# Performance work log

Hardware: AMD Instinct MI355X
Metric: run time of the kernel (lower is better)

The kernel has to match this reference:

```python
import jax, jax.numpy as jnp
import numpy as np

EC = 32        # pos-embed channels per coordinate (gno_embed_channels)
MAXP = 10000.0 # gno_embed_max_positions


def sin_embed(c):
    # c: [N, D] coords in [0,1] -> [N, D*EC] transformer-style sinusoidal embedding
    half = EC // 2
    freqs = MAXP ** (jnp.arange(half, dtype=jnp.float32) / half)
    ang = c[..., None] * freqs                       # [N, D, half]
    emb = jnp.concatenate([jnp.sin(ang), jnp.cos(ang)], axis=-1)  # [N, D, EC]
    return emb.reshape(c.shape[0], -1)


def mlp(h, layers):
    n = len(layers)
    for i, (W, b) in enumerate(layers):
        h = h @ W + b
        if i < n - 1:
            h = jax.nn.gelu(h)
    return h


def gno(y, xq, f_y, idx, layers, lift, reduction):
    # y: [n_y,3] source coords, xq: [n_x,3] query coords, f_y: [n_y,C_f], idx: [n_x,K]
    ye, xe = sin_embed(y), sin_embed(xq)
    K = idx.shape[1]
    ef = jnp.concatenate(
        [ye[idx], jnp.broadcast_to(xe[:, None, :], (xq.shape[0], K, xe.shape[-1]))], axis=-1)
    k = mlp(ef, layers)                              # [n_x, K, C] kernel values
    f = f_y if lift is None else f_y @ lift[0] + lift[1]
    msg = k * f[idx]                                 # gathered features modulated by kernel
    return msg.mean(axis=1) if reduction == 'mean' else msg.sum(axis=1)


def spectral_conv(v, w):
    # v: [1,X,Y,Z,C]; w: [4,m,m,m,C,C,2] (4 corner blocks, real/imag stacked)
    m = w.shape[2]
    wc = w[..., 0] + 1j * w[..., 1]
    vf = jnp.fft.rfftn(v, axes=(1, 2, 3))
    out = jnp.zeros_like(vf)
    corners = [(slice(0, m), slice(0, m)), (slice(0, m), slice(-m, None)),
               (slice(-m, None), slice(0, m)), (slice(-m, None), slice(-m, None))]
    for i, (sx, sy) in enumerate(corners):
        blk = jnp.einsum('bxyzi,xyzio->bxyzo', vf[:, sx, sy, :m, :], wc[i])
        out = out.at[:, sx, sy, :m, :].set(blk)
    return jnp.fft.irfftn(out, s=v.shape[1:4], axes=(1, 2, 3))


def _forward(input_geom, latent_queries, output_queries, x,
             in_lift_w, in_lift_b,
             in_k_w0, in_k_b0, in_k_w1, in_k_b1, in_k_w2, in_k_b2, in_k_w3, in_k_b3,
             lift_w0, lift_b0, lift_w1, lift_b1,
             spec_w, skip_w, gate_w, gate_b, cmlp_w0, cmlp_b0, cmlp_w1, cmlp_b1,
             out_k_w0, out_k_b0, out_k_w1, out_k_b1, out_k_w2, out_k_b2,
             proj_w0, proj_b0, proj_w1, proj_b1,
             in_idx, out_idx):
    grid = latent_queries.shape[:-1]
    flat_lq = latent_queries.reshape(-1, latent_queries.shape[-1])
    # --- input GNO: point cloud -> latent grid (mean reduction) ---
    in_layers = [(in_k_w0, in_k_b0), (in_k_w1, in_k_b1), (in_k_w2, in_k_b2), (in_k_w3, in_k_b3)]
    in_p = gno(input_geom, flat_lq, x, in_idx, in_layers, (in_lift_w, in_lift_b), 'mean')
    h = in_p.reshape((1,) + grid + (in_p.shape[-1],))
    # --- lifting ChannelMLP (2 layers) ---
    h = jax.nn.gelu(h @ lift_w0 + lift_b0) @ lift_w1 + lift_b1
    # --- FNO blocks ---
    for l in range(spec_w.shape[0]):
        v_fno = spectral_conv(h, spec_w[l])
        v_skip = h @ skip_w[l]                       # linear skip
        a = jax.nn.gelu(v_fno + v_skip)
        gate = a * gate_w[l] + gate_b[l]             # soft-gating skip
        m_ = jax.nn.gelu(a @ cmlp_w0[l] + cmlp_b0[l]) @ cmlp_w1[l] + cmlp_b1[l]
        h = jax.nn.gelu(m_ + gate)
    x_latent = h.reshape(-1, h.shape[-1])            # [nx*ny*nz, C]
    # --- output GNO: latent grid -> output queries (sum reduction) ---
    out_layers = [(out_k_w0, out_k_b0), (out_k_w1, out_k_b1), (out_k_w2, out_k_b2)]
    out_eval = gno(flat_lq, output_queries, x_latent, out_idx, out_layers, None, 'sum')
    out = out_eval[None]                             # [1, n_out, C]
    # --- projection ChannelMLP ---
    return jax.nn.gelu(out @ proj_w0 + proj_b0) @ proj_w1 + proj_b1


def setup_inputs() -> dict:
    key = jax.random.key(0)
    ks = jax.random.split(key, 24)
    N_IN, N_OUT, G, K = 100000, 30000, 32, 10
    C_IN, H = 3, 64
    KIN = 2 * 3 * EC  # 192: concat of two per-point embeddings

    def w(k, shape, fan):
        return jax.random.normal(k, shape, jnp.float32) / np.sqrt(fan)

    lin = jnp.linspace(0.0, 1.0, G)
    gx, gy, gz = jnp.meshgrid(lin, lin, lin, indexing='ij')
    d = {
        'input_geom': jax.random.uniform(ks[0], (N_IN, 3), jnp.float32),
        'latent_queries': jnp.stack([gx, gy, gz], axis=-1),
        'output_queries': jax.random.uniform(ks[1], (N_OUT, 3), jnp.float32),
        'x': jax.random.normal(ks[2], (N_IN, C_IN), jnp.float32),
        'in_lift_w': w(ks[3], (C_IN, H), C_IN), 'in_lift_b': jnp.zeros((H,)),
        'in_k_w0': w(ks[4], (KIN, 80), KIN), 'in_k_b0': jnp.zeros((80,)),
        'in_k_w1': w(ks[5], (80, 80), 80), 'in_k_b1': jnp.zeros((80,)),
        'in_k_w2': w(ks[6], (80, 80), 80), 'in_k_b2': jnp.zeros((80,)),
        'in_k_w3': w(ks[7], (80, H), 80), 'in_k_b3': jnp.zeros((H,)),
        'lift_w0': w(ks[8], (H, 128), H), 'lift_b0': jnp.zeros((128,)),
        'lift_w1': w(ks[9], (128, H), 128), 'lift_b1': jnp.zeros((H,)),
        'spec_w': jax.random.normal(ks[10], (4, 4, 8, 8, 8, H, H, 2), jnp.float32) * 0.02,
        'skip_w': w(ks[11], (4, H, H), H),
        'gate_w': jnp.ones((4, H)), 'gate_b': jnp.zeros((4, H)),
        'cmlp_w0': w(ks[12], (4, H, 128), H), 'cmlp_b0': jnp.zeros((4, 128)),
        'cmlp_w1': w(ks[13], (4, 128, H), 128), 'cmlp_b1': jnp.zeros((4, H)),
        'out_k_w0': w(ks[14], (KIN, 512), KIN), 'out_k_b0': jnp.zeros((512,)),
        'out_k_w1': w(ks[15], (512, 256), 512), 'out_k_b1': jnp.zeros((256,)),
        'out_k_w2': w(ks[16], (256, H), 256), 'out_k_b2': jnp.zeros((H,)),
        'proj_w0': w(ks[17], (H, 256), H), 'proj_b0': jnp.zeros((256,)),
        'proj_w1': w(ks[18], (256, 1), 256), 'proj_b1': jnp.zeros((1,)),
        'in_idx': jax.random.randint(ks[19], (G ** 3, K), 0, N_IN),
        'out_idx': jax.random.randint(ks[20], (N_OUT, K), 0, G ** 3),
    }
    return d


def reference(input_geom, latent_queries, output_queries, x,
              in_lift_w, in_lift_b,
              in_k_w0, in_k_b0, in_k_w1, in_k_b1, in_k_w2, in_k_b2, in_k_w3, in_k_b3,
              lift_w0, lift_b0, lift_w1, lift_b1,
              spec_w, skip_w, gate_w, gate_b, cmlp_w0, cmlp_b0, cmlp_w1, cmlp_b1,
              out_k_w0, out_k_b0, out_k_w1, out_k_b1, out_k_w2, out_k_b2,
              proj_w0, proj_b0, proj_w1, proj_b1,
              in_idx, out_idx):
    return _forward(input_geom, latent_queries, output_queries, x,
                    in_lift_w, in_lift_b,
                    in_k_w0, in_k_b0, in_k_w1, in_k_b1, in_k_w2, in_k_b2, in_k_w3, in_k_b3,
                    lift_w0, lift_b0, lift_w1, lift_b1,
                    spec_w, skip_w, gate_w, gate_b, cmlp_w0, cmlp_b0, cmlp_w1, cmlp_b1,
                    out_k_w0, out_k_b0, out_k_w1, out_k_b1, out_k_w2, out_k_b2,
                    proj_w0, proj_b0, proj_w1, proj_b1,
                    in_idx, out_idx)
```

## Files before the change

kernel.cpp:

```cpp
#include <hip/hip_runtime.h>
#include <math.h>

#define N_IN   100000
#define N_LQ   32768
#define N_OUT  30000
#define KNB    10

typedef _Float16 h8 __attribute__((ext_vector_type(8)));
typedef _Float16 h4 __attribute__((ext_vector_type(4)));
typedef float    v4f __attribute__((ext_vector_type(4)));

__device__ __forceinline__ float gelu_f(float x){
  float t = 0.79788456080286536f * (x + 0.044715f*x*x*x);
  t = fminf(fmaxf(t, -15.f), 15.f);
  float e = __expf(2.f*t);
  float th = __fdividef(e - 1.f, e + 1.f);
  return 0.5f*x*(1.f + th);
}

__global__ void k_twiddle(float* __restrict__ twc, float* __restrict__ tws){
  int t = threadIdx.x;
  if(t < 32){
    double a = (double)t * 0.19634954084936207;
    twc[t] = (float)cos(a);
    tws[t] = (float)sin(a);
  }
}

__global__ void k_prep(const float* __restrict__ okw1, const float* __restrict__ okw2,
                       const float* __restrict__ ikw1, const float* __restrict__ ikw2,
                       const float* __restrict__ ikw3,
                       _Float16* W1h, _Float16* W1l, _Float16* W2h, _Float16* W2l,
                       _Float16* I1h, _Float16* I1l, _Float16* I2h, _Float16* I2l,
                       _Float16* I3h, _Float16* I3l)
{
  int idx = blockIdx.x*256 + threadIdx.x;
  if(idx < 512*256){
    int k = idx>>8, n = idx&255;
    float v = okw1[idx];
    _Float16 hi = (_Float16)v;
    W1h[n*512+k] = hi; W1l[n*512+k] = (_Float16)((v-(float)hi)*2048.f);
  }
  if(idx < 256*64){
    int k = idx>>6, n = idx&63;
    float v = okw2[idx];
    _Float16 hi = (_Float16)v;
    W2h[n*256+k] = hi; W2l[n*256+k] = (_Float16)((v-(float)hi)*2048.f);
  }
  if(idx < 6400){
    int n = idx/80, k = idx - n*80;
    float v = ikw1[k*80+n];
    _Float16 hi = (_Float16)v;
    I1h[n*80+k] = hi; I1l[n*80+k] = (_Float16)((v-(float)hi)*2048.f);
    float v2 = ikw2[k*80+n];
    _Float16 hi2 = (_Float16)v2;
    I2h[n*80+k] = hi2; I2l[n*80+k] = (_Float16)((v2-(float)hi2)*2048.f);
  }
  if(idx < 5120){
    int n = idx/80, k = idx - n*80;
    float v = ikw3[k*64+n];
    _Float16 hi = (_Float16)v;
    I3h[n*80+k] = hi; I3l[n*80+k] = (_Float16)((v-(float)hi)*2048.f);
  }
}

__global__ void k_lift_in(const float* __restrict__ x, const float* __restrict__ w,
                          const float* __restrict__ b, float* __restrict__ f){
  int i = blockIdx.x*256 + threadIdx.x;
  if(i >= N_IN*64) return;
  int p = i>>6, c = i&63;
  float v = b[c];
  v = fmaf(x[p*3+0], w[c],      v);
  v = fmaf(x[p*3+1], w[64+c],   v);
  v = fmaf(x[p*3+2], w[128+c],  v);
  f[i] = v;
}

template<int COLS, bool BIAS>
__global__ __launch_bounds__(256) void k_embed_partial(
    const float* __restrict__ coords, int npts,
    const float* __restrict__ W, int roff,
    const float* __restrict__ bias, float* __restrict__ outp)
{
  __shared__ float emb[96*8];
  int p0 = blockIdx.x*8;
  int t  = threadIdx.x;
  for(int w = t; w < 384; w += 256){
    int pl = w / 48, s = w - pl*48;
    int d = s >> 4, fi = s & 15;
    int p = p0 + pl;
    float cd = (p < npts) ? coords[(size_t)p*3 + d] : 0.f;
    double f = exp((double)fi * 0.5756462732485115);
    double a = (double)cd * f;
    double sn, cs; sincos(a, &sn, &cs);
    emb[((d<<5)+fi)*8 + pl]      = (float)sn;
    emb[((d<<5)+16+fi)*8 + pl]   = (float)cs;
  }
  __syncthreads();
  for(int c = t; c < COLS; c += 256){
    float acc[8];
    float bb = BIAS ? bias[c] : 0.f;
    #pragma unroll
    for(int u=0;u<8;u++) acc[u] = bb;
    for(int i=0;i<96;i++){
      float wv = W[(size_t)(roff+i)*COLS + c];
      const float* ep = &emb[i*8];
      float4 e0 = *(const float4*)ep;
      float4 e1 = *(const float4*)(ep+4);
      acc[0]=fmaf(e0.x,wv,acc[0]); acc[1]=fmaf(e0.y,wv,acc[1]);
      acc[2]=fmaf(e0.z,wv,acc[2]); acc[3]=fmaf(e0.w,wv,acc[3]);
      acc[4]=fmaf(e1.x,wv,acc[4]); acc[5]=fmaf(e1.y,wv,acc[5]);
      acc[6]=fmaf(e1.z,wv,acc[6]); acc[7]=fmaf(e1.w,wv,acc[7]);
    }
    #pragma unroll
    for(int u=0;u<8;u++){
      int p = p0+u;
      if(p < npts) outp[(size_t)p*COLS + c] = acc[u];
    }
  }
}

#define GI_HAHI 0
#define GI_HALO 5632
#define GI_WHI  11264
#define GI_WLO  14464
__global__ __launch_bounds__(256,2) void k_gino(
    const float* __restrict__ Ain, const float* __restrict__ Bin,
    const float* __restrict__ f_in, const int* __restrict__ iidx,
    const _Float16* __restrict__ I1h, const _Float16* __restrict__ I1l, const float* __restrict__ b1,
    const _Float16* __restrict__ I2h, const _Float16* __restrict__ I2l, const float* __restrict__ b2,
    const _Float16* __restrict__ I3h, const _Float16* __restrict__ I3l, const float* __restrict__ b3,
    float* __restrict__ in_p)
{
  __shared__ _Float16 SG[17664];
  __shared__ int js[64]; __shared__ int qs[64];
  int t = threadIdx.x;
  int wid = t>>6, lane = t&63, quad = lane>>4, lm = lane&15;
  int et0 = blockIdx.x*64;
  if(t<64){ js[t] = iidx[et0+t]; qs[t] = (et0+t)/KNB; }
  __syncthreads();

  {
    int e = t>>2, k4 = t&3;
    size_t ja = (size_t)js[e]*80, qa = (size_t)qs[e]*80;
    #pragma unroll
    for(int u=0;u<3;u++){
      int kl = k4*8 + u*32;
      if(kl < 80){
        float4 a0 = *(const float4*)(Ain + ja + kl);
        float4 a1 = *(const float4*)(Ain + ja + kl + 4);
        float4 c0 = *(const float4*)(Bin + qa + kl);
        float4 c1 = *(const float4*)(Bin + qa + kl + 4);
        float vv[8] = {a0.x+c0.x, a0.y+c0.y, a0.z+c0.z, a0.w+c0.w,
                       a1.x+c1.x, a1.y+c1.y, a1.z+c1.z, a1.w+c1.w};
        h8 hh, ll;
        #pragma unroll
        for(int q8=0;q8<8;q8++){
          float g = gelu_f(vv[q8]);
          _Float16 hi = (_Float16)g;
          hh[q8] = hi; ll[q8] = (_Float16)((g-(float)hi)*2048.f);
        }
        *(h8*)&SG[GI_HAHI + e*88 + kl] = hh;
        *(h8*)&SG[GI_HALO + e*88 + kl] = ll;
      }
    }
  }

  const float inv = 4.8828125e-4f;
  const _Float16* whp[3] = {I1h, I2h, I3h};
  const _Float16* wlp[3] = {I1l, I2l, I3l};
  const float*    bsp[3] = {b1, b2, b3};
  v4f aH[5], aL[5];

  for(int l=0;l<3;l++){
    int NT = (l==2)?4:5;
    const _Float16* wh = whp[l];
    const _Float16* wl = wlp[l];
    #pragma unroll
    for(int n=0;n<5;n++){ aH[n] = (v4f)(0.f); aL[n] = (v4f)(0.f); }
    for(int c=0;c<3;c++){
      int kb = c*32;
      int per = (c==2)?2:4;
      int units = NT*16*per;
      __syncthreads();
      for(int u=t; u<units; u+=256){
        int n = u/per, kh = (u - n*per)*8;
        float4 rh = *(const float4*)(wh + n*80 + kb + kh);
        float4 rl = *(const float4*)(wl + n*80 + kb + kh);
        *(float4*)&SG[GI_WHI + n*40 + kh] = rh;
        *(float4*)&SG[GI_WLO + n*40 + kh] = rl;
      }
      __syncthreads();
      int arow = (wid*16+lm)*88;
      if(c<2){
        h8 ah = *(const h8*)&SG[GI_HAHI + arow + kb + quad*8];
        h8 al = *(const h8*)&SG[GI_HALO + arow + kb + quad*8];
        for(int n=0;n<NT;n++){
          int brow = (n*16+lm)*40;
          h8 bh = *(const h8*)&SG[GI_WHI + brow + quad*8];
          h8 bl = *(const h8*)&SG[GI_WLO + brow + quad*8];
          aH[n] = __builtin_amdgcn_mfma_f32_16x16x32_f16(ah, bh, aH[n], 0,0,0);
          aL[n] = __builtin_amdgcn_mfma_f32_16x16x32_f16(ah, bl, aL[n], 0,0,0);
          aL[n] = __builtin_amdgcn_mfma_f32_16x16x32_f16(al, bh, aL[n], 0,0,0);
        }
      } else {
        h4 ah = *(const h4*)&SG[GI_HAHI + arow + 64 + quad*4];
        h4 al = *(const h4*)&SG[GI_HALO + arow + 64 + quad*4];
        for(int n=0;n<NT;n++){
          int brow = (n*16+lm)*40;
          h4 bh = *(const h4*)&SG[GI_WHI + brow + quad*4];
          h4 bl = *(const h4*)&SG[GI_WLO + brow + quad*4];
          aH[n] = __builtin_amdgcn_mfma_f32_16x16x16f16(ah, bh, aH[n], 0,0,0);
          aL[n] = __builtin_amdgcn_mfma_f32_16x16x16f16(ah, bl, aL[n], 0,0,0);
          aL[n] = __builtin_amdgcn_mfma_f32_16x16x16f16(al, bh, aL[n], 0,0,0);
        }
      }
    }
    if(l<2){
      for(int n=0;n<NT;n++){
        float bb = bsp[l][n*16+lm];
        #pragma unroll
        for(int reg=0;reg<4;reg++){
          int e = wid*16 + quad*4 + reg;
          float v = aH[n][reg] + aL[n][reg]*inv + bb;
          v = gelu_f(v);
          _Float16 hi = (_Float16)v;
          SG[GI_HAHI + e*88 + n*16+lm] = hi;
          SG[GI_HALO + e*88 + n*16+lm] = (_Float16)((v-(float)hi)*2048.f);
        }
      }
    } else {
      for(int n=0;n<NT;n++){
        int col = n*16+lm;
        float bb = bsp[2][col];
        #pragma unroll
        for(int reg=0;reg<4;reg++){
          int e = wid*16 + quad*4 + reg;
          float v = aH[n][reg] + aL[n][reg]*inv + bb;
          v *= f_in[(size_t)js[e]*64 + col] * 0.1f;
          atomicAdd(&in_p[(size_t)qs[e]*64 + col], v);
        }
      }
    }
  }
}

#define OG_AHI  0
#define OG_ALO  2560
#define OG_BHI  5120
#define OG_BLO  15360
#define OG_W2HI 0
#define OG_W2LO 2560
#define OG_H1HI 5120
#define OG_H1LO 7680
__global__ __launch_bounds__(256,2) void k_ogno(
    const float* __restrict__ Aout, const float* __restrict__ Bout,
    const int* __restrict__ oidx,
    const _Float16* __restrict__ W1h, const _Float16* __restrict__ W1l,
    const float* __restrict__ b1,
    const _Float16* __restrict__ W2h, const _Float16* __restrict__ W2l,
    const float* __restrict__ b2,
    const float* __restrict__ xlat, float* __restrict__ outev, int eEnd)
{
  __shared__ _Float16 SH[25600];
  __shared__ int js[64]; __shared__ int qs[64];
  int t = threadIdx.x;
  int wid = t>>6, lane = t&63, quad = lane>>4, lm = lane&15;
  int et0 = blockIdx.x*64;
  if(t<64){
    int ec = et0+t; if(ec >= eEnd) ec = eEnd-1;
    js[t] = oidx[ec]; qs[t] = ec/KNB;
  }
  __syncthreads();

  v4f accH[4][4], accL[4][4];
  #pragma unroll
  for(int m=0;m<4;m++)
    #pragma unroll
    for(int n=0;n<4;n++){ accH[m][n] = (v4f)(0.f); accL[m][n] = (v4f)(0.f); }

  int se = t>>2, skl = (t&3)*8;
  size_t sja = (size_t)js[se]*512 + skl;
  size_t sqa = (size_t)qs[se]*512 + skl;

  for(int kk=0; kk<512; kk+=32){
    {
      const float* pa = Aout + sja + kk;
      const float* pb = Bout + sqa + kk;
      float4 a0 = *(const float4*)pa;
      float4 a1 = *(const float4*)(pa+4);
      float4 c0 = *(const float4*)pb;
      float4 c1 = *(const float4*)(pb+4);
      float vv[8] = {a0.x+c0.x, a0.y+c0.y, a0.z+c0.z, a0.w+c0.w,
                     a1.x+c1.x, a1.y+c1.y, a1.z+c1.z, a1.w+c1.w};
      h8 hh, ll;
      #pragma unroll
      for(int q8=0;q8<8;q8++){
        float g = gelu_f(vv[q8]);
        _Float16 hi = (_Float16)g;
        hh[q8] = hi; ll[q8] = (_Float16)((g-(float)hi)*2048.f);
      }
      *(h8*)&SH[OG_AHI + se*40 + skl] = hh;
      *(h8*)&SH[OG_ALO + se*40 + skl] = ll;
    }
    {
      const float4* ph = (const float4*)(W1h + (size_t)t*512 + kk);
      const float4* pl = (const float4*)(W1l + (size_t)t*512 + kk);
      float4 r0=ph[0], r1=ph[1], r2=ph[2], r3=ph[3];
      *(float4*)&SH[OG_BHI + t*40 +  0] = r0;
      *(float4*)&SH[OG_BHI + t*40 +  8] = r1;
      *(float4*)&SH[OG_BHI + t*40 + 16] = r2;
      *(float4*)&SH[OG_BHI + t*40 + 24] = r3;
      r0=pl[0]; r1=pl[1]; r2=pl[2]; r3=pl[3];
      *(float4*)&SH[OG_BLO + t*40 +  0] = r0;
      *(float4*)&SH[OG_BLO + t*40 +  8] = r1;
      *(float4*)&SH[OG_BLO + t*40 + 16] = r2;
      *(float4*)&SH[OG_BLO + t*40 + 24] = r3;
    }
    __syncthreads();
    h8 ah[4], al[4];
    #pragma unroll
    for(int m=0;m<4;m++){
      ah[m] = *(const h8*)&SH[OG_AHI + (m*16+lm)*40 + quad*8];
      al[m] = *(const h8*)&SH[OG_ALO + (m*16+lm)*40 + quad*8];
    }
    for(int n=0;n<4;n++){
      int nr = ((wid*4+n)*16+lm)*40 + quad*8;
      h8 bh = *(const h8*)&SH[OG_BHI + nr];
      h8 bl = *(const h8*)&SH[OG_BLO + nr];
      #pragma unroll
      for(int m=0;m<4;m++){
        accH[m][n] = __builtin_amdgcn_mfma_f32_16x16x32_f16(ah[m], bh, accH[m][n], 0,0,0);
        accL[m][n] = __builtin_amdgcn_mfma_f32_16x16x32_f16(ah[m], bl, accL[m][n], 0,0,0);
        accL[m][n] = __builtin_amdgcn_mfma_f32_16x16x32_f16(al[m], bh, accL[m][n], 0,0,0);
      }
    }
    __syncthreads();
  }

  const float inv = 4.8828125e-4f;
  v4f acc2H[4], acc2L[4];
  #pragma unroll
  for(int m=0;m<4;m++){ acc2H[m] = (v4f)(0.f); acc2L[m] = (v4f)(0.f); }

  for(int w2=0; w2<4; ++w2){
    for(int s=0; s<2; ++s){
      int ksub = w2*64 + s*32;
      {
        int n2 = t&63, kh = (t>>6)*8;
        float4 rh = *(const float4*)(W2h + (size_t)n2*256 + ksub + kh);
        float4 rl = *(const float4*)(W2l + (size_t)n2*256 + ksub + kh);
        *(float4*)&SH[OG_W2HI + n2*40 + kh] = rh;
        *(float4*)&SH[OG_W2LO + n2*40 + kh] = rl;
      }
      if(wid == w2){
        #pragma unroll
        for(int tt=0;tt<2;tt++){
          int n = 2*s+tt;
          float bb = b1[(w2*4+n)*16 + lm];
          #pragma unroll
          for(int m=0;m<4;m++){
            #pragma unroll
            for(int reg=0;reg<4;reg++){
              int e = m*16 + quad*4 + reg;
              float v = accH[m][n][reg] + accL[m][n][reg]*inv + bb;
              v = gelu_f(v);
              _Float16 hi = (_Float16)v;
              SH[OG_H1HI + e*40 + tt*16 + lm] = hi;
              SH[OG_H1LO + e*40 + tt*16 + lm] = (_Float16)((v-(float)hi)*2048.f);
            }
          }
        }
      }
      __syncthreads();
      h8 bh = *(const h8*)&SH[OG_W2HI + (wid*16+lm)*40 + quad*8];
      h8 bl = *(const h8*)&SH[OG_W2LO + (wid*16+lm)*40 + quad*8];
      #pragma unroll
      for(int m=0;m<4;m++){
        h8 a2h = *(const h8*)&SH[OG_H1HI + (m*16+lm)*40 + quad*8];
        h8 a2l = *(const h8*)&SH[OG_H1LO + (m*16+lm)*40 + quad*8];
        acc2H[m] = __builtin_amdgcn_mfma_f32_16x16x32_f16(a2h, bh, acc2H[m], 0,0,0);
        acc2L[m] = __builtin_amdgcn_mfma_f32_16x16x32_f16(a2h, bl, acc2L[m], 0,0,0);
        acc2L[m] = __builtin_amdgcn_mfma_f32_16x16x32_f16(a2l, bh, acc2L[m], 0,0,0);
      }
      __syncthreads();
    }
  }

  int n2 = wid*16 + lm;
  float bb2 = b2[n2];
  #pragma unroll
  for(int m=0;m<4;m++){
    #pragma unroll
    for(int reg=0;reg<4;reg++){
      int e = m*16 + quad*4 + reg;
      int eg = et0 + e;
      if(eg < eEnd){
        float v = acc2H[m][reg] + acc2L[m][reg]*inv + bb2;
        v *= xlat[(size_t)js[e]*64 + n2];
        atomicAdd(&outev[(size_t)qs[e]*64 + n2], v);
      }
    }
  }
}

__global__ __launch_bounds__(256) void k_mlp_plain(const float* __restrict__ X,
    const float* __restrict__ W0, const float* __restrict__ b0,
    const float* __restrict__ W1, const float* __restrict__ b1,
    float* __restrict__ Y)
{
  __shared__ float xt[64*16];
  __shared__ float ht[128*16];
  int t = threadIdx.x, r0 = blockIdx.x*16;
  for(int w=t; w<1024; w+=256){ int r=w>>6, c=w&63; xt[c*16+r] = X[(size_t)(r0+r)*64+c]; }
  __syncthreads();
  {
    int hc = t & 127, rg = t >> 7;
    float acc[8]; float bb = b0[hc];
    #pragma unroll
    for(int u=0;u<8;u++) acc[u]=bb;
    for(int i=0;i<64;i++){
      float wv = W0[i*128+hc];
      const float* xp = &xt[i*16 + rg*8];
      float4 x0 = *(const float4*)xp; float4 x1 = *(const float4*)(xp+4);
      acc[0]=fmaf(x0.x,wv,acc[0]); acc[1]=fmaf(x0.y,wv,acc[1]);
      acc[2]=fmaf(x0.z,wv,acc[2]); acc[3]=fmaf(x0.w,wv,acc[3]);
      acc[4]=fmaf(x1.x,wv,acc[4]); acc[5]=fmaf(x1.y,wv,acc[5]);
      acc[6]=fmaf(x1.z,wv,acc[6]); acc[7]=fmaf(x1.w,wv,acc[7]);
    }
    #pragma unroll
    for(int u=0;u<8;u++) ht[hc*16 + rg*8 + u] = gelu_f(acc[u]);
  }
  __syncthreads();
  {
    int oc = t & 63, rg = t >> 6;
    float acc2[4]; float bb = b1[oc];
    #pragma unroll
    for(int u=0;u<4;u++) acc2[u]=bb;
    for(int i=0;i<128;i++){
      float wv = W1[i*64+oc];
      float4 h4v = *(const float4*)&ht[i*16 + rg*4];
      acc2[0]=fmaf(h4v.x,wv,acc2[0]); acc2[1]=fmaf(h4v.y,wv,acc2[1]);
      acc2[2]=fmaf(h4v.z,wv,acc2[2]); acc2[3]=fmaf(h4v.w,wv,acc2[3]);
    }
    #pragma unroll
    for(int u=0;u<4;u++) Y[(size_t)(r0+rg*4+u)*64 + oc] = acc2[u];
  }
}

__global__ __launch_bounds__(256) void k_mlp_gated(const float* __restrict__ X,
    const float* __restrict__ W0, const float* __restrict__ b0,
    const float* __restrict__ W1, const float* __restrict__ b1,
    const float* __restrict__ gwp, const float* __restrict__ gbp,
    float* __restrict__ Y)
{
  __shared__ float xt[64*16];
  __shared__ float ht[128*16];
  int t = threadIdx.x, r0 = blockIdx.x*16;
  for(int w=t; w<1024; w+=256){ int r=w>>6, c=w&63; xt[c*16+r] = X[(size_t)(r0+r)*64+c]; }
  __syncthreads();
  {
    int hc = t & 127, rg = t >> 7;
    float acc[8]; float bb = b0[hc];
    #pragma unroll
    for(int u=0;u<8;u++) acc[u]=bb;
    for(int i=0;i<64;i++){
      float wv = W0[i*128+hc];
      const float* xp = &xt[i*16 + rg*8];
      float4 x0 = *(const float4*)xp; float4 x1 = *(const float4*)(xp+4);
      acc[0]=fmaf(x0.x,wv,acc[0]); acc[1]=fmaf(x0.y,wv,acc[1]);
      acc[2]=fmaf(x0.z,wv,acc[2]); acc[3]=fmaf(x0.w,wv,acc[3]);
      acc[4]=fmaf(x1.x,wv,acc[4]); acc[5]=fmaf(x1.y,wv,acc[5]);
      acc[6]=fmaf(x1.z,wv,acc[6]); acc[7]=fmaf(x1.w,wv,acc[7]);
    }
    #pragma unroll
    for(int u=0;u<8;u++) ht[hc*16 + rg*8 + u] = gelu_f(acc[u]);
  }
  __syncthreads();
  {
    int oc = t & 63, rg = t >> 6;
    float acc2[4]; float bb = b1[oc];
    #pragma unroll
    for(int u=0;u<4;u++) acc2[u]=bb;
    for(int i=0;i<128;i++){
      float wv = W1[i*64+oc];
      float4 h4v = *(const float4*)&ht[i*16 + rg*4];
      acc2[0]=fmaf(h4v.x,wv,acc2[0]); acc2[1]=fmaf(h4v.y,wv,acc2[1]);
      acc2[2]=fmaf(h4v.z,wv,acc2[2]); acc2[3]=fmaf(h4v.w,wv,acc2[3]);
    }
    float gwv = gwp[oc], gbv = gbp[oc];
    #pragma unroll
    for(int u=0;u<4;u++){
      int r = rg*4+u;
      float a = xt[oc*16 + r];
      Y[(size_t)(r0+r)*64 + oc] = gelu_f(acc2[u] + fmaf(a, gwv, gbv));
    }
  }
}

__global__ void k_fz_fwd(const float* __restrict__ h, const float* __restrict__ twc,
                         const float* __restrict__ tws, float* __restrict__ Fr, float* __restrict__ Fi){
  int idx = blockIdx.x*256 + threadIdx.x;
  int c = idx&63, kz=(idx>>6)&7, y=(idx>>9)&31, x=idx>>14;
  const float* hp = h + ((size_t)(x*32+y)*32)*64 + c;
  float re=0.f, im=0.f;
  for(int z=0; z<32; z++){
    float v = hp[(size_t)z*64];
    int k = (kz*z)&31;
    re = fmaf(v, twc[k], re);
    im = fmaf(-v, tws[k], im);
  }
  Fr[idx]=re; Fi[idx]=im;
}

__global__ void k_fy_fwd(const float* __restrict__ Ar, const float* __restrict__ Ai,
                         const float* __restrict__ twc, const float* __restrict__ tws,
                         float* __restrict__ Fr, float* __restrict__ Fi){
  int idx = blockIdx.x*256 + threadIdx.x;
  int c = idx&63, kz=(idx>>6)&7, my=(idx>>9)&15, x=idx>>13;
  int ky = my<8 ? my : my+16;
  const float* pr = Ar + ((size_t)(x*32)*8+kz)*64 + c;
  const float* pi = Ai + ((size_t)(x*32)*8+kz)*64 + c;
  float re=0.f, im=0.f;
  for(int y=0;y<32;y++){
    float a = pr[(size_t)y*512], b = pi[(size_t)y*512];
    int k = (ky*y)&31; float cs=twc[k], sn=tws[k];
    re += a*cs + b*sn;
    im += b*cs - a*sn;
  }
  Fr[idx]=re; Fi[idx]=im;
}

__global__ void k_fx_fwd(const float* __restrict__ Ar, const float* __restrict__ Ai,
                         const float* __restrict__ twc, const float* __restrict__ tws,
                         float* __restrict__ Fr, float* __restrict__ Fi){
  int idx = blockIdx.x*256 + threadIdx.x;
  int c = idx&63, kz=(idx>>6)&7, my=(idx>>9)&15, mx=idx>>13;
  int kx = mx<8 ? mx : mx+16;
  const float* pr = Ar + ((size_t)my*8+kz)*64 + c;
  const float* pi = Ai + ((size_t)my*8+kz)*64 + c;
  float re=0.f, im=0.f;
  for(int x=0;x<32;x++){
    float a = pr[(size_t)x*8192], b = pi[(size_t)x*8192];
    int k = (kx*x)&31; float cs=twc[k], sn=tws[k];
    re += a*cs + b*sn;
    im += b*cs - a*sn;
  }
  Fr[idx]=re; Fi[idx]=im;
}

__global__ void k_smm(const float* __restrict__ Fr, const float* __restrict__ Fi,
                      const float* __restrict__ wlayer,
                      float* __restrict__ Gr, float* __restrict__ Gi){
  int t = threadIdx.x;
  int sub = t>>6, c = t&63;
  int mp = blockIdx.x*4 + sub;
  int kz = mp&7, my=(mp>>3)&15, mx=mp>>7;
  int corner = ((mx>=8)?2:0) | ((my>=8)?1:0);
  int kxp = mx&7, kyp = my&7;
  const float* wp = wlayer + (size_t)(((corner*8+kxp)*8+kyp)*8+kz)*8192;
  __shared__ float fre[4][64], fim[4][64];
  fre[sub][c] = Fr[(size_t)mp*64+c];
  fim[sub][c] = Fi[(size_t)mp*64+c];
  __syncthreads();
  float are=0.f, aim=0.f;
  for(int i=0;i<64;i++){
    float2 wv = *(const float2*)&wp[(size_t)(i*64+c)*2];
    float a = fre[sub][i], b = fim[sub][i];
    are += a*wv.x - b*wv.y;
    aim += a*wv.y + b*wv.x;
  }
  Gr[(size_t)mp*64+c] = are;
  Gi[(size_t)mp*64+c] = aim;
}

__global__ void k_fx_inv(const float* __restrict__ Ar, const float* __restrict__ Ai,
                         const float* __restrict__ twc, const float* __restrict__ tws,
                         float* __restrict__ Fr, float* __restrict__ Fi){
  int idx = blockIdx.x*256 + threadIdx.x;
  int c = idx&63, kz=(idx>>6)&7, my=(idx>>9)&15, x=idx>>13;
  float re=0.f, im=0.f;
  for(int mx=0;mx<16;mx++){
    int kx = mx<8 ? mx : mx+16;
    int k = (kx*x)&31; float cs=twc[k], sn=tws[k];
    float a = Ar[(size_t)((mx*16+my)*8+kz)*64+c];
    float b = Ai[(size_t)((mx*16+my)*8+kz)*64+c];
    re += a*cs - b*sn;
    im += a*sn + b*cs;
  }
  Fr[idx]=re; Fi[idx]=im;
}

__global__ void k_fy_inv(const float* __restrict__ Ar, const float* __restrict__ Ai,
                         const float* __restrict__ twc, const float* __restrict__ tws,
                         float* __restrict__ Fr, float* __restrict__ Fi){
  int idx = blockIdx.x*256 + threadIdx.x;
  int c = idx&63, kz=(idx>>6)&7, y=(idx>>9)&31, x=idx>>14;
  float re=0.f, im=0.f;
  for(int my=0;my<16;my++){
    int ky = my<8 ? my : my+16;
    int k = (ky*y)&31; float cs=twc[k], sn=tws[k];
    float a = Ar[(size_t)((x*16+my)*8+kz)*64+c];
    float b = Ai[(size_t)((x*16+my)*8+kz)*64+c];
    re += a*cs - b*sn;
    im += a*sn + b*cs;
  }
  Fr[idx]=re; Fi[idx]=im;
}

__global__ void k_fz_inv_skip(const float* __restrict__ G2re, const float* __restrict__ G2im,
    const float* __restrict__ h, const float* __restrict__ twc, const float* __restrict__ tws,
    const float* __restrict__ sw, float* __restrict__ a_out)
{
  __shared__ float hrow[4][64];
  int t = threadIdx.x; int c = t&63; int pl = t>>6;
  int p = blockIdx.x*4 + pl;
  int z = p & 31; int xy = p >> 5;
  hrow[pl][c] = h[(size_t)p*64 + c];
  __syncthreads();
  const float* gr = G2re + (size_t)(xy*8)*64 + c;
  const float* gi = G2im + (size_t)(xy*8)*64 + c;
  float acc = gr[0];
  #pragma unroll
  for(int kz=1;kz<8;kz++){
    int k = (kz*z)&31;
    acc += 2.f*(gr[(size_t)kz*64]*twc[k] - gi[(size_t)kz*64]*tws[k]);
  }
  float vfno = acc * (1.f/32768.f);
  float vskip = 0.f;
  for(int i=0;i<64;i++) vskip = fmaf(hrow[pl][i], sw[i*64+c], vskip);
  a_out[(size_t)p*64+c] = gelu_f(vfno + vskip);
}

__global__ __launch_bounds__(256) void k_proj(const float* __restrict__ outev,
    const float* __restrict__ pw0, const float* __restrict__ pb0,
    const float* __restrict__ pw1, const float* __restrict__ pb1,
    float* __restrict__ outp)
{
  __shared__ float msg[8][64];
  __shared__ float red[8][4];
  int t = threadIdx.x; int q0 = blockIdx.x*8;
  for(int w=t; w<512; w+=256){
    int qq=w>>6, o=w&63; int q=q0+qq;
    msg[qq][o] = (q<N_OUT) ? outev[(size_t)q*64+o] : 0.f;
  }
  __syncthreads();
  float p[8]; float bb = pb0[t];
  #pragma unroll
  for(int qq=0;qq<8;qq++) p[qq]=bb;
  for(int o=0;o<64;o++){
    float wv = pw0[o*256+t];
    #pragma unroll
    for(int qq=0;qq<8;qq++) p[qq] = fmaf(msg[qq][o], wv, p[qq]);
  }
  float w1v = pw1[t];
  int lane = t & 63, wid = t >> 6;
  #pragma unroll
  for(int qq=0;qq<8;qq++){
    float v = gelu_f(p[qq]) * w1v;
    for(int d=32; d>=1; d>>=1) v += __shfl_down(v, d, 64);
    if(lane==0) red[qq][wid]=v;
  }
  __syncthreads();
  if(t<8){
    int q = q0+t;
    if(q<N_OUT) outp[q] = red[t][0]+red[t][1]+red[t][2]+red[t][3] + pb1[0];
  }
}

extern "C" void kernel_launch(void* const* d_in, const int* in_sizes, int n_in,
                              void* d_out, int out_size, void* d_ws, size_t ws_size,
                              hipStream_t stream)
{
  (void)in_sizes; (void)n_in; (void)out_size; (void)ws_size;
  const float* geom = (const float*)d_in[0];
  const float* latq = (const float*)d_in[1];
  const float* outq = (const float*)d_in[2];
  const float* xin  = (const float*)d_in[3];
  const float* ilw  = (const float*)d_in[4];
  const float* ilb  = (const float*)d_in[5];
  const float* ikw0 = (const float*)d_in[6];
  const float* ikb0 = (const float*)d_in[7];
  const float* ikw1 = (const float*)d_in[8];
  const float* ikb1 = (const float*)d_in[9];
  const float* ikw2 = (const float*)d_in[10];
  const float* ikb2 = (const float*)d_in[11];
  const float* ikw3 = (const float*)d_in[12];
  const float* ikb3 = (const float*)d_in[13];
  const float* lw0  = (const float*)d_in[14];
  const float* lb0  = (const float*)d_in[15];
  const float* lw1  = (const float*)d_in[16];
  const float* lb1  = (const float*)d_in[17];
  const float* specw= (const float*)d_in[18];
  const float* skw  = (const float*)d_in[19];
  const float* gw   = (const float*)d_in[20];
  const float* gb   = (const float*)d_in[21];
  const float* cw0  = (const float*)d_in[22];
  const float* cb0  = (const float*)d_in[23];
  const float* cw1  = (const float*)d_in[24];
  const float* cb1  = (const float*)d_in[25];
  const float* okw0 = (const float*)d_in[26];
  const float* okb0 = (const float*)d_in[27];
  const float* okw1 = (const float*)d_in[28];
  const float* okb1 = (const float*)d_in[29];
  const float* okw2 = (const float*)d_in[30];
  const float* okb2 = (const float*)d_in[31];
  const float* pw0  = (const float*)d_in[32];
  const float* pb0  = (const float*)d_in[33];
  const float* pw1  = (const float*)d_in[34];
  const float* pb1  = (const float*)d_in[35];
  const int* iidx = (const int*)d_in[36];
  const int* oidx = (const int*)d_in[37];
  float* outp = (float*)d_out;
  float* ws = (float*)d_ws;

  size_t off = 0;
  float* F_IN = ws + off; off += (size_t)N_IN*64;
  float* AIN  = ws + off; off += (size_t)N_IN*80;
  float* BIN_ = ws + off; off += (size_t)N_LQ*80;
  float* AOUT = ws + off; off += (size_t)N_LQ*512;
  float* BOUT = ws + off; off += (size_t)N_OUT*512;
  float* HBUF = ws + off; off += (size_t)N_LQ*64;
  float* ABUF = ws + off; off += (size_t)N_LQ*64;
  float* FZr = ws+off; off+=524288; float* FZi = ws+off; off+=524288;
  float* FYr = ws+off; off+=262144; float* FYi = ws+off; off+=262144;
  float* FXr = ws+off; off+=131072; float* FXi = ws+off; off+=131072;
  float* GMr = ws+off; off+=131072; float* GMi = ws+off; off+=131072;
  float* G1r = ws+off; off+=262144; float* G1i = ws+off; off+=262144;
  float* G2r = ws+off; off+=524288; float* G2i = ws+off; off+=524288;
  float* OUTEV = ws+off; off += (size_t)N_OUT*64;
  float* TWC = ws+off; off+=32; float* TWS = ws+off; off+=32;
  off = (off + 3) & ~(size_t)3;
  _Float16* P = (_Float16*)(ws + off);
  _Float16 *W1h = P,          *W1l = P+131072;
  _Float16 *W2h = P+262144,   *W2l = P+278528;
  _Float16 *I1h = P+294912,   *I1l = P+301312;
  _Float16 *I2h = P+307712,   *I2l = P+314112;
  _Float16 *I3h = P+320512,   *I3l = P+325632;

  k_twiddle<<<1, 64, 0, stream>>>(TWC, TWS);
  k_prep<<<512, 256, 0, stream>>>(okw1, okw2, ikw1, ikw2, ikw3,
                                  W1h, W1l, W2h, W2l, I1h, I1l, I2h, I2l, I3h, I3l);
  k_lift_in<<<(N_IN*64)/256, 256, 0, stream>>>(xin, ilw, ilb, F_IN);
  k_embed_partial<80,false><<<N_IN/8, 256, 0, stream>>>(geom, N_IN, ikw0, 0, (const float*)nullptr, AIN);
  k_embed_partial<80,true ><<<N_LQ/8, 256, 0, stream>>>(latq, N_LQ, ikw0, 96, ikb0, BIN_);
  k_embed_partial<512,false><<<N_LQ/8, 256, 0, stream>>>(latq, N_LQ, okw0, 0, (const float*)nullptr, AOUT);
  k_embed_partial<512,true ><<<(N_OUT+7)/8, 256, 0, stream>>>(outq, N_OUT, okw0, 96, okb0, BOUT);

  hipMemsetAsync(HBUF, 0, (size_t)N_LQ*64*sizeof(float), stream);
  k_gino<<<(N_LQ*KNB)/64, 256, 0, stream>>>(AIN, BIN_, F_IN, iidx,
                                            I1h, I1l, ikb1, I2h, I2l, ikb2, I3h, I3l, ikb3, HBUF);
  k_mlp_plain<<<N_LQ/16, 256, 0, stream>>>(HBUF, lw0, lb0, lw1, lb1, HBUF);

  for(int l=0;l<4;l++){
    k_fz_fwd<<<2048,256,0,stream>>>(HBUF, TWC, TWS, FZr, FZi);
    k_fy_fwd<<<1024,256,0,stream>>>(FZr, FZi, TWC, TWS, FYr, FYi);
    k_fx_fwd<<<512,256,0,stream>>>(FYr, FYi, TWC, TWS, FXr, FXi);
    k_smm<<<512,256,0,stream>>>(FXr, FXi, specw + (size_t)l*16777216, GMr, GMi);
    k_fx_inv<<<1024,256,0,stream>>>(GMr, GMi, TWC, TWS, G1r, G1i);
    k_fy_inv<<<2048,256,0,stream>>>(G1r, G1i, TWC, TWS, G2r, G2i);
    k_fz_inv_skip<<<8192,256,0,stream>>>(G2r, G2i, HBUF, TWC, TWS, skw + (size_t)l*4096, ABUF);
    k_mlp_gated<<<N_LQ/16,256,0,stream>>>(ABUF, cw0 + (size_t)l*8192, cb0 + l*128,
                                          cw1 + (size_t)l*8192, cb1 + l*64,
                                          gw + l*64, gb + l*64, HBUF);
  }

  hipMemsetAsync(OUTEV, 0, (size_t)N_OUT*64*sizeof(float), stream);
  k_ogno<<<(N_OUT*KNB + 63)/64, 256, 0, stream>>>(AOUT, BOUT, oidx,
                                                  W1h, W1l, okb1, W2h, W2l, okb2,
                                                  HBUF, OUTEV, N_OUT*KNB);
  k_proj<<<(N_OUT+7)/8, 256, 0, stream>>>(OUTEV, pw0, pb0, pw1, pb1, outp);
}
```

Measured before the change: 1.957 ms.

## Restructure output GNO kernel: direct global weight loads, prefetch gather, single-pass layer-2

In k_ogno, the W1 hi/lo tiles are no longer staged through shared memory; each wave reads its B fragments directly from global memory. The gathered A/B rows for the next K-chunk are prefetched into registers before the barrier, so the gather latency overlaps the MFMA work. The GELU'd layer-1 activations are written once to a larger LDS buffer, and layer 2 runs in one pass with W2 fragments read from global, replacing the per-wave serialized loop with its many barriers. This trades LDS staging and barriers for more global/L2 traffic on the weights and a larger LDS footprint, which may reduce occupancy. The A tile LDS stride drops from padded 40 to unpadded 32, which may add bank conflicts.

```diff
diff --git a/kernel.cpp b/kernel.cpp
--- a/kernel.cpp
+++ b/kernel.cpp
@@ -245,14 +245,6 @@
   }
 }
 
-#define OG_AHI  0
-#define OG_ALO  2560
-#define OG_BHI  5120
-#define OG_BLO  15360
-#define OG_W2HI 0
-#define OG_W2LO 2560
-#define OG_H1HI 5120
-#define OG_H1LO 7680
 __global__ __launch_bounds__(256,2) void k_ogno(
     const float* __restrict__ Aout, const float* __restrict__ Bout,
     const int* __restrict__ oidx,
@@ -262,7 +254,7 @@
     const float* __restrict__ b2,
     const float* __restrict__ xlat, float* __restrict__ outev, int eEnd)
 {
-  __shared__ _Float16 SH[25600];
+  __shared__ _Float16 SH[33792];
   __shared__ int js[64]; __shared__ int qs[64];
   int t = threadIdx.x;
   int wid = t>>6, lane = t&63, quad = lane>>4, lm = lane&15;
@@ -280,19 +272,19 @@
     for(int n=0;n<4;n++){ accH[m][n] = (v4f)(0.f); accL[m][n] = (v4f)(0.f); }
 
   int se = t>>2, skl = (t&3)*8;
-  size_t sja = (size_t)js[se]*512 + skl;
-  size_t sqa = (size_t)qs[se]*512 + skl;
-
+  const float* pa = Aout + (size_t)js[se]*512 + skl;
+  const float* pb = Bout + (size_t)qs[se]*512 + skl;
+
+  float4 cA0 = *(const float4*)(pa);
+  float4 cA1 = *(const float4*)(pa+4);
+  float4 cB0 = *(const float4*)(pb);
+  float4 cB1 = *(const float4*)(pb+4);
+
+  #pragma unroll 1
   for(int kk=0; kk<512; kk+=32){
     {
-      const float* pa = Aout + sja + kk;
-      const float* pb = Bout + sqa + kk;
-      float4 a0 = *(const float4*)pa;
-      float4 a1 = *(const float4*)(pa+4);
-      float4 c0 = *(const float4*)pb;
-      float4 c1 = *(const float4*)(pb+4);
-      float vv[8] = {a0.x+c0.x, a0.y+c0.y, a0.z+c0.z, a0.w+c0.w,
-                     a1.x+c1.x, a1.y+c1.y, a1.z+c1.z, a1.w+c1.w};
+      float vv[8] = {cA0.x+cB0.x, cA0.y+cB0.y, cA0.z+cB0.z, cA0.w+cB0.w,
+                     cA1.x+cB1.x, cA1.y+cB1.y, cA1.z+cB1.z, cA1.w+cB1.w};
       h8 hh, ll;
       #pragma unroll
       for(int q8=0;q8<8;q8++){
@@ -300,94 +292,86 @@
         _Float16 hi = (_Float16)g;
         hh[q8] = hi; ll[q8] = (_Float16)((g-(float)hi)*2048.f);
       }
-      *(h8*)&SH[OG_AHI + se*40 + skl] = hh;
-      *(h8*)&SH[OG_ALO + se*40 + skl] = ll;
-    }
-    {
-      const float4* ph = (const float4*)(W1h + (size_t)t*512 + kk);
-      const float4* pl = (const float4*)(W1l + (size_t)t*512 + kk);
-      float4 r0=ph[0], r1=ph[1], r2=ph[2], r3=ph[3];
-      *(float4*)&SH[OG_BHI + t*40 +  0] = r0;
-      *(float4*)&SH[OG_BHI + t*40 +  8] = r1;
-      *(float4*)&SH[OG_BHI + t*40 + 16] = r2;
-      *(float4*)&SH[OG_BHI + t*40 + 24] = r3;
-      r0=pl[0]; r1=pl[1]; r2=pl[2]; r3=pl[3];
-      *(float4*)&SH[OG_BLO + t*40 +  0] = r0;
-      *(float4*)&SH[OG_BLO + t*40 +  8] = r1;
-      *(float4*)&SH[OG_BLO + t*40 + 16] = r2;
-      *(float4*)&SH[OG_BLO + t*40 + 24] = r3;
+      *(h8*)&SH[se*32 + skl] = hh;
+      *(h8*)&SH[2048 + se*32 + skl] = ll;
+    }
+    if(kk < 480){
+      cA0 = *(const float4*)(pa + kk + 32);
+      cA1 = *(const float4*)(pa + kk + 36);
+      cB0 = *(const float4*)(pb + kk + 32);
+      cB1 = *(const float4*)(pb + kk + 36);
     }
     __syncthreads();
-    h8 ah[4], al[4];
+    h8 ah[4], al[4], bh[4], bl[4];
     #pragma unroll
     for(int m=0;m<4;m++){
-      ah[m] = *(const h8*)&SH[OG_AHI + (m*16+lm)*40 + quad*8];
-      al[m] = *(const h8*)&SH[OG_ALO + (m*16+lm)*40 + quad*8];
-    }
+      ah[m] = *(const h8*)&SH[(m*16+lm)*32 + quad*8];
+      al[m] = *(const h8*)&SH[2048 + (m*16+lm)*32 + quad*8];
+    }
+    #pragma unroll
     for(int n=0;n<4;n++){
-      int nr = ((wid*4+n)*16+lm)*40 + quad*8;
-      h8 bh = *(const h8*)&SH[OG_BHI + nr];
-      h8 bl = *(const h8*)&SH[OG_BLO + nr];
+      size_t off = (size_t)((wid*4+n)*16+lm)*512 + kk + quad*8;
+      bh[n] = *(const h8*)(W1h + off);
+      bl[n] = *(const h8*)(W1l + off);
+    }
+    #pragma unroll
+    for(int n=0;n<4;n++)
       #pragma unroll
-      for(int m=0;m<4;m++){
-        accH[m][n] = __builtin_amdgcn_mfma_f32_16x16x32_f16(ah[m], bh, accH[m][n], 0,0,0);
-        accL[m][n] = __builtin_amdgcn_mfma_f32_16x16x32_f16(ah[m], bl, accL[m][n], 0,0,0);
-        accL[m][n] = __builtin_amdgcn_mfma_f32_16x16x32_f16(al[m], bh, accL[m][n], 0,0,0);
+      for(int m=0;m<4;m++)
+        accH[m][n] = __builtin_amdgcn_mfma_f32_16x16x32_f16(ah[m], bh[n], accH[m][n], 0,0,0);
+    #pragma unroll
+    for(int n=0;n<4;n++)
+      #pragma unroll
+      for(int m=0;m<4;m++)
+        accL[m][n] = __builtin_amdgcn_mfma_f32_16x16x32_f16(ah[m], bl[n], accL[m][n], 0,0,0);
+    #pragma unroll
+    for(int n=0;n<4;n++)
+      #pragma unroll
+      for(int m=0;m<4;m++)
+        accL[m][n] = __builtin_amdgcn_mfma_f32_16x16x32_f16(al[m], bh[n], accL[m][n], 0,0,0);
+    __syncthreads();
+  }
+
+  const float inv = 4.8828125e-4f;
+  #pragma unroll
+  for(int n=0;n<4;n++){
+    int col = (wid*4+n)*16 + lm;
+    float bb = b1[col];
+    #pragma unroll
+    for(int m=0;m<4;m++){
+      #pragma unroll
+      for(int reg=0;reg<4;reg++){
+        int e = m*16 + quad*4 + reg;
+        float v = accH[m][n][reg] + accL[m][n][reg]*inv + bb;
+        v = gelu_f(v);
+        _Float16 hi = (_Float16)v;
+        SH[e*264 + col] = hi;
+        SH[16896 + e*264 + col] = (_Float16)((v-(float)hi)*2048.f);
       }
     }
-    __syncthreads();
-  }
-
-  const float inv = 4.8828125e-4f;
+  }
+  __syncthreads();
+
   v4f acc2H[4], acc2L[4];
   #pragma unroll
   for(int m=0;m<4;m++){ acc2H[m] = (v4f)(0.f); acc2L[m] = (v4f)(0.f); }
-
-  for(int w2=0; w2<4; ++w2){
-    for(int s=0; s<2; ++s){
-      int ksub = w2*64 + s*32;
-      {
-        int n2 = t&63, kh = (t>>6)*8;
-        float4 rh = *(const float4*)(W2h + (size_t)n2*256 + ksub + kh);
-        float4 rl = *(const float4*)(W2l + (size_t)n2*256 + ksub + kh);
-        *(float4*)&SH[OG_W2HI + n2*40 + kh] = rh;
-        *(float4*)&SH[OG_W2LO + n2*40 + kh] = rl;
-      }
-      if(wid == w2){
-        #pragma unroll
-        for(int tt=0;tt<2;tt++){
-          int n = 2*s+tt;
-          float bb = b1[(w2*4+n)*16 + lm];
-          #pragma unroll
-          for(int m=0;m<4;m++){
-            #pragma unroll
-            for(int reg=0;reg<4;reg++){
-              int e = m*16 + quad*4 + reg;
-              float v = accH[m][n][reg] + accL[m][n][reg]*inv + bb;
-              v = gelu_f(v);
-              _Float16 hi = (_Float16)v;
-              SH[OG_H1HI + e*40 + tt*16 + lm] = hi;
-              SH[OG_H1LO + e*40 + tt*16 + lm] = (_Float16)((v-(float)hi)*2048.f);
-            }
-          }
-        }
-      }
-      __syncthreads();
-      h8 bh = *(const h8*)&SH[OG_W2HI + (wid*16+lm)*40 + quad*8];
-      h8 bl = *(const h8*)&SH[OG_W2LO + (wid*16+lm)*40 + quad*8];
-      #pragma unroll
-      for(int m=0;m<4;m++){
-        h8 a2h = *(const h8*)&SH[OG_H1HI + (m*16+lm)*40 + quad*8];
-        h8 a2l = *(const h8*)&SH[OG_H1LO + (m*16+lm)*40 + quad*8];
-        acc2H[m] = __builtin_amdgcn_mfma_f32_16x16x32_f16(a2h, bh, acc2H[m], 0,0,0);
-        acc2L[m] = __builtin_amdgcn_mfma_f32_16x16x32_f16(a2h, bl, acc2L[m], 0,0,0);
-        acc2L[m] = __builtin_amdgcn_mfma_f32_16x16x32_f16(a2l, bh, acc2L[m], 0,0,0);
-      }
-      __syncthreads();
-    }
-  }
-
   int n2 = wid*16 + lm;
+  #pragma unroll
+  for(int c=0;c<8;c++){
+    int ksub = c*32;
+    size_t woff = (size_t)n2*256 + ksub + quad*8;
+    h8 bh2 = *(const h8*)(W2h + woff);
+    h8 bl2 = *(const h8*)(W2l + woff);
+    #pragma unroll
+    for(int m=0;m<4;m++){
+      h8 a2h = *(const h8*)&SH[(m*16+lm)*264 + ksub + quad*8];
+      h8 a2l = *(const h8*)&SH[16896 + (m*16+lm)*264 + ksub + quad*8];
+      acc2H[m] = __builtin_amdgcn_mfma_f32_16x16x32_f16(a2h, bh2, acc2H[m], 0,0,0);
+      acc2L[m] = __builtin_amdgcn_mfma_f32_16x16x32_f16(a2h, bl2, acc2L[m], 0,0,0);
+      acc2L[m] = __builtin_amdgcn_mfma_f32_16x16x32_f16(a2l, bh2, acc2L[m], 0,0,0);
+    }
+  }
+
   float bb2 = b2[n2];
   #pragma unroll
   for(int m=0;m<4;m++){
```

Result: faster. 1.861 ms (-4.9%).
